# Kernel tuning notes

Measured on AMD Instinct MI355X. Metric: run time of the kernel, lower is better.

## Reference

```python
import jax, jax.numpy as jnp
import numpy as np

B, NE, NN, L = 64, 256, 1024, 512
F_IN, HID = 128, 128
VOCAB = 50000
ALPHA = 0.2
NEG = -9.0e15


def _leaky(z):
    return jnp.where(z >= 0, z, ALPHA * z)


def hga_layer(x, adj, W, W2, W3, a, a2, wc, transfer, concat):
    # x: [B, NN, Fin], adj: [B, NE, NN] (hyperedge incidence)
    O = W2.shape[1]
    x4 = x @ W2                      # [B, NN, O]
    if transfer:
        x = x @ W                    # [B, NN, O]
    # node->edge attention: score depends only on node k (query is shared word_context)
    s0 = wc[0] @ a[:O, 0]            # scalar
    e1 = _leaky(x4 @ a[O:, 0] + s0)  # [B, NN]
    e1 = jnp.broadcast_to(e1[:, None, :], adj.shape)          # [B, NE, NN]
    att_edge = jax.nn.softmax(jnp.where(adj > 0, e1, NEG), axis=2)
    edge = att_edge @ x              # [B, NE, O]
    edge4 = edge @ W3                # [B, NE, O]
    # edge->node attention: query = node feat x4[k], key = edge feat edge4[j]
    e2 = _leaky((x4 @ a2[:O, 0])[:, None, :] + (edge4 @ a2[O:, 0])[:, :, None])  # [B, NE, NN]
    att_node = jax.nn.softmax(jnp.where(adj > 0, e2, NEG).transpose(0, 2, 1), axis=2)  # [B, NN, NE]
    node = att_node @ edge           # [B, NN, O]
    return jax.nn.elu(node) if concat else node


def setup_inputs() -> dict:
    key = jax.random.key(0)
    ks = jax.random.split(key, 16)
    stdv = 1.0 / np.sqrt(HID)
    u = lambda k, shape: jax.random.uniform(k, shape, jnp.float32, -stdv, stdv)
    inp = {
        "items": jax.random.randint(ks[0], (B, NN), 0, VOCAB),
        "alias_inputs": jax.random.randint(ks[1], (B, L), 0, NN),
        "node_masks": jnp.ones((B, L), jnp.float32),
        "adj": jax.random.randint(ks[2], (B, NE, NN), 0, 2).astype(jnp.float32),
        "emb": jax.random.normal(ks[3], (VOCAB, F_IN), jnp.float32),
        # layer 1 (transfer=False, concat=True)
        "w2_1": u(ks[4], (F_IN, HID)),
        "w3_1": u(ks[5], (HID, HID)),
        "a_1": u(ks[6], (2 * HID, 1)),
        "a2_1": u(ks[7], (2 * HID, 1)),
        "wc_1": u(ks[8], (1, HID)),
        # layer 2 (transfer=True, concat=False)
        "w_2": u(ks[9], (HID, HID)),
        "w2_2": u(ks[10], (HID, HID)),
        "w3_2": u(ks[11], (HID, HID)),
        "a_2": u(ks[12], (2 * HID, 1)),
        "a2_2": u(ks[13], (2 * HID, 1)),
        "wc_2": u(ks[14], (1, HID)),
        "ln_g": jnp.ones((HID,), jnp.float32),
        "ln_b": jnp.zeros((HID,), jnp.float32),
    }
    return inp


def reference(items, alias_inputs, node_masks, adj, emb,
              w2_1, w3_1, a_1, a2_1, wc_1,
              w_2, w2_2, w3_2, a_2, a2_2, wc_2,
              ln_g, ln_b):
    hidden = emb[items]                                        # [B, NN, F]
    x = hga_layer(hidden, adj, None, w2_1, w3_1, a_1, a2_1, wc_1,
                  transfer=False, concat=True)
    x = hga_layer(x, adj, w_2, w2_2, w3_2, a_2, a2_2, wc_2,
                  transfer=True, concat=False)                 # [B, NN, HID]
    seq = jnp.take_along_axis(x, alias_inputs[:, :, None], axis=1)  # [B, L, HID]
    m = node_masks[:, :, None]
    h = seq * m
    b = jnp.sum(h * m, axis=-2) / jnp.sum(node_masks, -1, keepdims=True)  # [B, HID]
    mu = jnp.mean(b, -1, keepdims=True)
    var = jnp.mean((b - mu) ** 2, -1, keepdims=True)
    return (b - mu) / jnp.sqrt(var + 1e-6) * ln_g + ln_b
```

## Files before the change

kernel.cpp:

```cpp
#include <hip/hip_runtime.h>
#include <hip/hip_bf16.h>

typedef __hip_bfloat16 bf16;
typedef __attribute__((ext_vector_type(8))) unsigned short u16x8;
typedef __attribute__((ext_vector_type(4))) unsigned short u16x4;
typedef __attribute__((ext_vector_type(4))) float f32x4;
typedef __attribute__((ext_vector_type(8))) short bf16x8;
typedef __attribute__((ext_vector_type(16))) unsigned char u8x16;

#define B_   64
#define NE_  256
#define NN_  1024
#define L_   512
#define HID_ 128
#define ALPHA_ 0.2f

__device__ __forceinline__ float bfu(unsigned short u){
  unsigned int x = ((unsigned int)u) << 16;
  union { unsigned int i; float f; } c; c.i = x; return c.f;
}
__device__ __forceinline__ unsigned short f2b(float f){
  bf16 h = __float2bfloat16(f);
  union { bf16 b; unsigned short u; } c; c.b = h; return c.u;
}
__device__ __forceinline__ int swz(int r, int c){ return (c ^ (r & 3) ^ ((r >> 2) & 3)) & 3; }

__global__ void k_consts(const float* w2_1, const float* w3_1,
                         const float* a_1, const float* a2_1, const float* wc_1,
                         const float* w2_2, const float* w3_2,
                         const float* a_2, const float* a2_2, const float* wc_2,
                         const float* w_2,
                         float* consts, unsigned short* W2T)
{
  int blk = blockIdx.x, t = threadIdx.x;
  __shared__ float red[128];
  if (blk < 6) {
    const float* M; const float* v;
    switch (blk) {
      case 0: M = w2_1; v = a_1  + 128; break;
      case 1: M = w2_1; v = a2_1;       break;
      case 2: M = w3_1; v = a2_1 + 128; break;
      case 3: M = w2_2; v = a_2  + 128; break;
      case 4: M = w2_2; v = a2_2;       break;
      default: M = w3_2; v = a2_2 + 128; break;
    }
    float acc = 0.f;
    for (int o = 0; o < 128; ++o) acc += M[t*128 + o] * v[o];
    consts[blk*128 + t] = acc;
  } else if (blk < 8) {
    const float* wc = (blk == 6) ? wc_1 : wc_2;
    const float* a  = (blk == 6) ? a_1  : a_2;
    red[t] = wc[t] * a[t];
    __syncthreads();
    for (int s = 64; s > 0; s >>= 1) { if (t < s) red[t] += red[t + s]; __syncthreads(); }
    if (t == 0) consts[768 + (blk - 6)] = red[0];
  } else {
    for (int k = 0; k < 128; ++k) W2T[t*128 + k] = f2b(w_2[k*128 + t]);
  }
}

__global__ void k_prep(const float* __restrict__ adj,
                       unsigned char* __restrict__ ADJB, unsigned char* __restrict__ ADJT)
{
  __shared__ unsigned char tile[64][68];
  int b  = blockIdx.z;
  int e0 = blockIdx.y * 64;
  int n0 = blockIdx.x * 64;
  int t  = threadIdx.x;
  int lr = t >> 2, lc0 = (t & 3) * 16;
  const float* src = adj + ((long)b*NE_ + e0 + lr)*NN_ + n0 + lc0;
  u8x16 ov;
  #pragma unroll
  for (int j = 0; j < 16; j += 4) {
    f32x4 v = *(const f32x4*)(src + j);
    #pragma unroll
    for (int k = 0; k < 4; ++k) {
      unsigned char u = (v[k] != 0.f) ? 1 : 0;
      ov[j+k] = u; tile[lr][lc0+j+k] = u;
    }
  }
  *(u8x16*)(ADJB + ((long)b*NE_ + e0 + lr)*NN_ + n0 + lc0) = ov;
  __syncthreads();
  u8x16 o;
  #pragma unroll
  for (int j = 0; j < 16; ++j) o[j] = tile[lc0 + j][lr];
  *(u8x16*)(ADJT + ((long)b*NN_ + n0 + lr)*NE_ + e0 + lc0) = o;
}

template<int SRCBF>
__global__ void k_fproj(const float* __restrict__ srcF, const unsigned short* __restrict__ srcB,
                        const int* __restrict__ gitems,
                        const float* __restrict__ consts, int layer,
                        float* __restrict__ w1, float* __restrict__ f1,
                        unsigned short* __restrict__ YT)
{
  __shared__ float ce1s[128], cf1s[128];
  __shared__ __attribute__((aligned(16))) unsigned short T[64][132];
  int b = blockIdx.y, n0 = blockIdx.x * 64, t = threadIdx.x;
  if (t < 128) { ce1s[t] = consts[layer*384 + t]; cf1s[t] = consts[layer*384 + 128 + t]; }
  __syncthreads();
  int r = t >> 2, h0 = (t & 3) * 32;
  long row = (long)b*NN_ + n0 + r;
  float s0 = consts[768 + layer];
  float xv[32];
  if (SRCBF) {
    const unsigned short* sp = srcB + row*HID_ + h0;
    #pragma unroll
    for (int j = 0; j < 32; j += 8) {
      u16x8 v = *(const u16x8*)(sp + j);
      #pragma unroll
      for (int k = 0; k < 8; ++k) xv[j+k] = bfu(v[k]);
    }
  } else {
    const float* sp = srcF + (long)gitems[row]*HID_ + h0;
    #pragma unroll
    for (int j = 0; j < 32; j += 4) {
      f32x4 v = *(const f32x4*)(sp + j);
      #pragma unroll
      for (int k = 0; k < 4; ++k) xv[j+k] = v[k];
    }
  }
  float p1 = 0.f, p2 = 0.f;
  #pragma unroll
  for (int j = 0; j < 32; ++j) { p1 += xv[j]*ce1s[h0+j]; p2 += xv[j]*cf1s[h0+j]; }
  p1 += __shfl_xor(p1, 1, 4); p1 += __shfl_xor(p1, 2, 4);
  p2 += __shfl_xor(p2, 1, 4); p2 += __shfl_xor(p2, 2, 4);
  float z = p1 + s0; z = (z >= 0.f) ? z : ALPHA_*z;
  float w = __expf(z);
  if ((t & 3) == 0) { w1[row] = w; f1[row] = p2; }
  #pragma unroll
  for (int j = 0; j < 32; j += 4) {
    u16x4 o;
    #pragma unroll
    for (int k = 0; k < 4; ++k) o[k] = f2b(w * xv[j+k]);
    *(u16x4*)&T[r][h0+j] = o;
  }
  __syncthreads();
  int h = t >> 1, nh = (t & 1) * 32;
  unsigned short* dst = YT + ((long)b*HID_ + h)*NN_ + n0 + nh;
  #pragma unroll
  for (int j = 0; j < 32; j += 8) {
    u16x8 o;
    #pragma unroll
    for (int k = 0; k < 8; ++k) o[k] = T[nh+j+k][h];
    *(u16x8*)&dst[j] = o;
  }
}

template<int TRANSFER>
__global__ __launch_bounds__(256) void k_gemm_edge(
    const unsigned char* __restrict__ ADJB,
    const unsigned short* __restrict__ YT,
    const float* __restrict__ w1v,
    const float* __restrict__ consts, int layer,
    const unsigned short* __restrict__ W2T,
    unsigned short* __restrict__ ET,
    float* __restrict__ f2o)
{
  __shared__ __attribute__((aligned(16))) unsigned short SM[12288];
  __shared__ float dsum[64];
  const int id = blockIdx.x;
  const int b = id & 63;
  const long e0 = (long)(id >> 6) * 64;
  const int t = threadIdx.x;
  const int lane = t & 63;
  const int w = t >> 6, wm = w >> 1, wn = w & 1;
  const int r4 = t >> 2, c4 = t & 3;
  const int lr = lane & 15, g = lane >> 4;

  f32x4 acc[2][4];
  #pragma unroll
  for (int i = 0; i < 2; ++i)
    #pragma unroll
    for (int j = 0; j < 4; ++j) acc[i][j] = (f32x4){0.f,0.f,0.f,0.f};

  const unsigned char*  Ab = ADJB + ((long)b*NE_ + e0 + r4)*NN_;
  const unsigned short* Bb = YT + (long)b*HID_*NN_;
  const float*          wb = w1v + (long)b*NN_;

  unsigned long aw; u16x8 bv0, bv1; f32x4 wv0, wv1;
  float dot = 0.f;

  auto stage = [&](int kc) {
    aw  = *(const unsigned long*)(Ab + kc + c4*8);
    wv0 = *(const f32x4*)(wb + kc + c4*8);
    wv1 = *(const f32x4*)(wb + kc + c4*8 + 4);
    bv0 = *(const u16x8*)(Bb + (long)r4*NN_ + kc + c4*8);
    bv1 = *(const u16x8*)(Bb + (long)(64+r4)*NN_ + kc + c4*8);
  };
  auto commit = [&](int buf) {
    u16x8 av;
    #pragma unroll
    for (int j = 0; j < 8; ++j) {
      unsigned int by = (unsigned int)(aw >> (8*j)) & 0xffu;
      av[j] = by ? (unsigned short)0x3F80 : (unsigned short)0;
      float wj = (j < 4) ? wv0[j] : wv1[j-4];
      dot += by ? wj : 0.f;
    }
    *(u16x8*)&SM[buf*2048 + r4*32 + swz(r4,c4)*8] = av;
    *(u16x8*)&SM[4096 + buf*4096 + r4*32 + swz(r4,c4)*8] = bv0;
    *(u16x8*)&SM[4096 + buf*4096 + (64+r4)*32 + swz(64+r4,c4)*8] = bv1;
  };

  stage(0); commit(0);
  int cur = 0;
  const int NIT = NN_/32;
  for (int it = 0; it < NIT; ++it) {
    __syncthreads();
    if (it+1 < NIT) stage((it+1)*32);
    const unsigned short* AsB = &SM[cur*2048];
    const unsigned short* BsB = &SM[4096 + cur*4096];
    bf16x8 af[2], bfr[4];
    #pragma unroll
    for (int mt = 0; mt < 2; ++mt) {
      int r = wm*32 + mt*16 + lr;
      af[mt] = *(const bf16x8*)&AsB[r*32 + swz(r,g)*8];
    }
    #pragma unroll
    for (int nt = 0; nt < 4; ++nt) {
      int n = wn*64 + nt*16 + lr;
      bfr[nt] = *(const bf16x8*)&BsB[n*32 + swz(n,g)*8];
    }
    #pragma unroll
    for (int mt = 0; mt < 2; ++mt)
      #pragma unroll
      for (int nt = 0; nt < 4; ++nt)
        acc[mt][nt] = __builtin_amdgcn_mfma_f32_16x16x32_bf16(af[mt], bfr[nt], acc[mt][nt], 0, 0, 0);
    if (it+1 < NIT) { commit(cur^1); cur ^= 1; }
  }
  dot += __shfl_down(dot, 2, 4); dot += __shfl_down(dot, 1, 4);
  if ((lane & 3) == 0) dsum[r4] = dot;
  __syncthreads();
  #pragma unroll
  for (int mt = 0; mt < 2; ++mt)
    #pragma unroll
    for (int nt = 0; nt < 4; ++nt) {
      int col = wn*64 + nt*16 + lr;
      #pragma unroll
      for (int q = 0; q < 4; ++q) {
        int rl = wm*32 + mt*16 + g*4 + q;
        SM[rl*136 + col] = f2b(acc[mt][nt][q] / dsum[rl]);
      }
    }
  __syncthreads();
  if (TRANSFER) {
    f32x4 acc2[2][4];
    #pragma unroll
    for (int i = 0; i < 2; ++i)
      #pragma unroll
      for (int j = 0; j < 4; ++j) acc2[i][j] = (f32x4){0.f,0.f,0.f,0.f};
    #pragma unroll
    for (int kc2 = 0; kc2 < 4; ++kc2) {
      bf16x8 af[2], bfr[4];
      #pragma unroll
      for (int mt = 0; mt < 2; ++mt) {
        int r = wm*32 + mt*16 + lr;
        af[mt] = *(const bf16x8*)&SM[r*136 + kc2*32 + g*8];
      }
      #pragma unroll
      for (int nt = 0; nt < 4; ++nt) {
        int n = wn*64 + nt*16 + lr;
        bfr[nt] = *(const bf16x8*)(W2T + n*128 + kc2*32 + g*8);
      }
      #pragma unroll
      for (int mt = 0; mt < 2; ++mt)
        #pragma unroll
        for (int nt = 0; nt < 4; ++nt)
          acc2[mt][nt] = __builtin_amdgcn_mfma_f32_16x16x32_bf16(af[mt], bfr[nt], acc2[mt][nt], 0, 0, 0);
    }
    __syncthreads();
    #pragma unroll
    for (int mt = 0; mt < 2; ++mt)
      #pragma unroll
      for (int nt = 0; nt < 4; ++nt) {
        int col = wn*64 + nt*16 + lr;
        #pragma unroll
        for (int q = 0; q < 4; ++q) {
          int rl = wm*32 + mt*16 + g*4 + q;
          SM[rl*136 + col] = f2b(acc2[mt][nt][q]);
        }
      }
    __syncthreads();
  }
  {
    const float* cf2 = consts + layer*384 + 256;
    int r = t >> 2, h0 = (t & 3) * 32;
    float p = 0.f;
    #pragma unroll
    for (int j = 0; j < 32; ++j) p += bfu(SM[r*136 + h0 + j]) * cf2[h0 + j];
    p += __shfl_down(p, 2, 4); p += __shfl_down(p, 1, 4);
    if ((t & 3) == 0) f2o[(long)b*NE_ + e0 + r] = p;
  }
  {
    int h = t >> 1, eh = (t & 1) * 32;
    unsigned short* dst = ET + ((long)b*HID_ + h)*NE_ + e0 + eh;
    #pragma unroll
    for (int j = 0; j < 32; j += 8) {
      u16x8 o;
      #pragma unroll
      for (int k = 0; k < 8; ++k) o[k] = SM[(eh+j+k)*136 + h];
      *(u16x8*)&dst[j] = o;
    }
  }
}

template<int EPI>
__global__ __launch_bounds__(256, 2) void k_gemm_att(
    const unsigned char* __restrict__ ADJT,
    const unsigned short* __restrict__ ET,
    const float* __restrict__ f1v, const float* __restrict__ f2v,
    unsigned short* __restrict__ X2,
    const float* __restrict__ wcount, float* __restrict__ pooled)
{
  __shared__ __attribute__((aligned(16))) unsigned short SM[12288];
  __shared__ float dsum[64];
  __shared__ float colsum[128];
  const int id = blockIdx.x;
  const int b = id & 63;
  const long m0 = (long)(id >> 6) * 64;
  const int t = threadIdx.x;
  const int lane = t & 63;
  const int w = t >> 6, wm = w >> 1, wn = w & 1;
  const int r4 = t >> 2, c4 = t & 3;
  const int lr = lane & 15, g = lane >> 4;

  f32x4 acc[2][4];
  #pragma unroll
  for (int i = 0; i < 2; ++i)
    #pragma unroll
    for (int j = 0; j < 4; ++j) acc[i][j] = (f32x4){0.f,0.f,0.f,0.f};

  const float f1r = f1v[(long)b*NN_ + m0 + r4];
  const unsigned char*  Ab = ADJT + ((long)b*NN_ + m0 + r4)*NE_;
  const unsigned short* Bb = ET + (long)b*HID_*NE_;
  const float* f2p = f2v + (long)b*NE_;

  unsigned long aw; u16x8 bv0, bv1; f32x4 fv0, fv1;
  float dot = 0.f;

  auto stage = [&](int kc) {
    aw  = *(const unsigned long*)(Ab + kc + c4*8);
    fv0 = *(const f32x4*)(f2p + kc + c4*8);
    fv1 = *(const f32x4*)(f2p + kc + c4*8 + 4);
    bv0 = *(const u16x8*)(Bb + (long)r4*NE_ + kc + c4*8);
    bv1 = *(const u16x8*)(Bb + (long)(64+r4)*NE_ + kc + c4*8);
  };
  auto commit = [&](int buf) {
    u16x8 av;
    #pragma unroll
    for (int j = 0; j < 8; ++j) {
      unsigned int by = (unsigned int)(aw >> (8*j)) & 0xffu;
      float z = f1r + ((j < 4) ? fv0[j] : fv1[j-4]);
      z = (z >= 0.f) ? z : ALPHA_ * z;
      float wt = by ? __expf(z) : 0.f;
      unsigned short us = f2b(wt);
      av[j] = us; dot += bfu(us);
    }
    *(u16x8*)&SM[buf*2048 + r4*32 + swz(r4,c4)*8] = av;
    *(u16x8*)&SM[4096 + buf*4096 + r4*32 + swz(r4,c4)*8] = bv0;
    *(u16x8*)&SM[4096 + buf*4096 + (64+r4)*32 + swz(64+r4,c4)*8] = bv1;
  };

  stage(0); commit(0);
  int cur = 0;
  const int NIT = NE_/32;
  for (int it = 0; it < NIT; ++it) {
    __syncthreads();
    if (it+1 < NIT) stage((it+1)*32);
    const unsigned short* AsB = &SM[cur*2048];
    const unsigned short* BsB = &SM[4096 + cur*4096];
    bf16x8 af[2], bfr[4];
    #pragma unroll
    for (int mt = 0; mt < 2; ++mt) {
      int r = wm*32 + mt*16 + lr;
      af[mt] = *(const bf16x8*)&AsB[r*32 + swz(r,g)*8];
    }
    #pragma unroll
    for (int nt = 0; nt < 4; ++nt) {
      int n = wn*64 + nt*16 + lr;
      bfr[nt] = *(const bf16x8*)&BsB[n*32 + swz(n,g)*8];
    }
    #pragma unroll
    for (int mt = 0; mt < 2; ++mt)
      #pragma unroll
      for (int nt = 0; nt < 4; ++nt)
        acc[mt][nt] = __builtin_amdgcn_mfma_f32_16x16x32_bf16(af[mt], bfr[nt], acc[mt][nt], 0, 0, 0);
    if (it+1 < NIT) { commit(cur^1); cur ^= 1; }
  }
  dot += __shfl_down(dot, 2, 4); dot += __shfl_down(dot, 1, 4);
  if ((lane & 3) == 0) dsum[r4] = dot;
  if (EPI == 2 && t < 128) colsum[t] = 0.f;
  __syncthreads();

  if (EPI == 1) {
    #pragma unroll
    for (int mt = 0; mt < 2; ++mt)
      #pragma unroll
      for (int nt = 0; nt < 4; ++nt) {
        int col = wn*64 + nt*16 + lr;
        #pragma unroll
        for (int q = 0; q < 4; ++q) {
          int rl = wm*32 + mt*16 + g*4 + q;
          float v = acc[mt][nt][q] / dsum[rl];
          v = (v > 0.f) ? v : expm1f(v);
          X2[(long)b*NN_*HID_ + (m0 + rl)*HID_ + col] = f2b(v);
        }
      }
  } else {
    float psum[4] = {0.f, 0.f, 0.f, 0.f};
    #pragma unroll
    for (int mt = 0; mt < 2; ++mt)
      #pragma unroll
      for (int q = 0; q < 4; ++q) {
        int rl = wm*32 + mt*16 + g*4 + q;
        float wc = wcount[(long)b*NN_ + m0 + rl];
        float inv = wc / dsum[rl];
        #pragma unroll
        for (int nt = 0; nt < 4; ++nt) psum[nt] += inv * acc[mt][nt][q];
      }
    #pragma unroll
    for (int nt = 0; nt < 4; ++nt) atomicAdd(&colsum[wn*64 + nt*16 + lr], psum[nt]);
    __syncthreads();
    if (t < 128) atomicAdd(&pooled[(long)b*HID_ + t], colsum[t]);
  }
}

__global__ void k_zero(float* __restrict__ p, int n)
{
  int i = blockIdx.x*256 + threadIdx.x;
  if (i < n) p[i] = 0.f;
}

__global__ void k_wcount(const int* __restrict__ alias, const float* __restrict__ masks,
                         float* __restrict__ wcount, float* __restrict__ msum)
{
  int b = blockIdx.x, t = threadIdx.x;
  float m = masks[b*L_ + t];
  int idx = alias[b*L_ + t];
  atomicAdd(&wcount[(long)b*NN_ + idx], m*m);
  float s = m;
  #pragma unroll
  for (int sh = 32; sh > 0; sh >>= 1) s += __shfl_down(s, sh);
  __shared__ float red[8];
  if ((t & 63) == 0) red[t >> 6] = s;
  __syncthreads();
  if (t == 0) { float tot = 0.f; for (int i = 0; i < 8; ++i) tot += red[i]; msum[b] = tot; }
}

__global__ void k_ln(const float* __restrict__ pooled, const float* __restrict__ msum,
                     const float* __restrict__ ln_g, const float* __restrict__ ln_b,
                     float* __restrict__ out)
{
  int b = blockIdx.x, t = threadIdx.x;
  __shared__ float sr[2];
  float bv = pooled[b*HID_ + t] / msum[b];
  int lane = t & 63;
  float p = bv;
  #pragma unroll
  for (int s = 32; s > 0; s >>= 1) p += __shfl_xor(p, s);
  if (lane == 0) sr[t >> 6] = p;
  __syncthreads();
  float mu = (sr[0] + sr[1]) * (1.f / HID_);
  float dv = bv - mu;
  p = dv * dv;
  #pragma unroll
  for (int s = 32; s > 0; s >>= 1) p += __shfl_xor(p, s);
  __syncthreads();
  if (lane == 0) sr[t >> 6] = p;
  __syncthreads();
  float var = (sr[0] + sr[1]) * (1.f / HID_);
  out[b*HID_ + t] = dv / sqrtf(var + 1e-6f) * ln_g[t] + ln_b[t];
}

extern "C" void kernel_launch(void* const* d_in, const int* in_sizes, int n_in,
                              void* d_out, int out_size, void* d_ws, size_t ws_size,
                              hipStream_t stream)
{
  const int*   items = (const int*)d_in[0];
  const int*   alias = (const int*)d_in[1];
  const float* masks = (const float*)d_in[2];
  const float* adj   = (const float*)d_in[3];
  const float* emb   = (const float*)d_in[4];
  const float* w2_1  = (const float*)d_in[5];
  const float* w3_1  = (const float*)d_in[6];
  const float* a_1   = (const float*)d_in[7];
  const float* a2_1  = (const float*)d_in[8];
  const float* wc_1  = (const float*)d_in[9];
  const float* w_2   = (const float*)d_in[10];
  const float* w2_2  = (const float*)d_in[11];
  const float* w3_2  = (const float*)d_in[12];
  const float* a_2   = (const float*)d_in[13];
  const float* a2_2  = (const float*)d_in[14];
  const float* wc_2  = (const float*)d_in[15];
  const float* ln_g  = (const float*)d_in[16];
  const float* ln_b  = (const float*)d_in[17];
  float* out = (float*)d_out;

  char* ws = (char*)d_ws;
  size_t off = 0;
  auto alloc = [&](size_t bytes) -> void* {
    void* p = ws + off; off += (bytes + 255) / 256 * 256; return p;
  };
  unsigned char*  ADJB = (unsigned char*) alloc((size_t)B_*NE_*NN_);
  unsigned char*  ADJT = (unsigned char*) alloc((size_t)B_*NN_*NE_);
  unsigned short* YT   = (unsigned short*)alloc((size_t)B_*HID_*NN_*2);
  unsigned short* ET   = (unsigned short*)alloc((size_t)B_*HID_*NE_*2);
  unsigned short* X2BF = (unsigned short*)alloc((size_t)B_*NN_*HID_*2);
  float* wcount= (float*)alloc((size_t)B_*NN_*4);
  float* pooled= (float*)alloc((size_t)B_*HID_*4);
  float* w1    = (float*)alloc((size_t)B_*NN_*4);
  float* f1    = (float*)alloc((size_t)B_*NN_*4);
  float* f2    = (float*)alloc((size_t)B_*NE_*4);
  float* msum  = (float*)alloc(B_*4);
  float* consts= (float*)alloc(772*4);
  unsigned short* W2T = (unsigned short*)alloc((size_t)HID_*HID_*2);
  if (off > ws_size) return;

  const int kZeroN = B_*NN_ + B_*HID_;

  k_consts<<<9, 128, 0, stream>>>(w2_1, w3_1, a_1, a2_1, wc_1, w2_2, w3_2, a_2, a2_2, wc_2,
                                  w_2, consts, W2T);
  k_zero<<<(kZeroN + 255)/256, 256, 0, stream>>>(wcount, kZeroN);
  k_wcount<<<B_, L_, 0, stream>>>(alias, masks, wcount, msum);
  k_prep<<<dim3(NN_/64, NE_/64, B_), 256, 0, stream>>>(adj, ADJB, ADJT);

  k_fproj<0><<<dim3(NN_/64, B_), 256, 0, stream>>>(emb, nullptr, items, consts, 0, w1, f1, YT);
  k_gemm_edge<0><<<B_*(NE_/64), 256, 0, stream>>>(ADJB, YT, w1, consts, 0, W2T, ET, f2);
  k_gemm_att<1><<<B_*(NN_/64), 256, 0, stream>>>(ADJT, ET, f1, f2, X2BF, nullptr, nullptr);

  k_fproj<1><<<dim3(NN_/64, B_), 256, 0, stream>>>(nullptr, X2BF, nullptr, consts, 1, w1, f1, YT);
  k_gemm_edge<1><<<B_*(NE_/64), 256, 0, stream>>>(ADJB, YT, w1, consts, 1, W2T, ET, f2);
  k_gemm_att<2><<<B_*(NN_/64), 256, 0, stream>>>(ADJT, ET, f1, f2, nullptr, wcount, pooled);

  k_ln<<<B_, HID_, 0, stream>>>(pooled, msum, ln_g, ln_b, out);
}
```

Baseline: 140.3 us.

## Bit-pack adjacency masks and fuse layer-2 projection into attention epilogue

Adjacency incidence is stored as packed bitmasks instead of one byte per entry, shrinking the mask traffic in the prep kernel and both GEMM stages. The layer-2 feature projection (weights, f1 scores, transposed weighted features) is computed directly in the layer-1 node-attention epilogue from shared memory, removing the intermediate bf16 node tensor round trip and one kernel launch. This adds an extra shared-memory pass and syncs to the epilogue, and it uses separate w1/f1 buffers per layer.

```diff
diff --git a/kernel.cpp b/kernel.cpp
--- a/kernel.cpp
+++ b/kernel.cpp
@@ -6,7 +6,6 @@
 typedef __attribute__((ext_vector_type(4))) unsigned short u16x4;
 typedef __attribute__((ext_vector_type(4))) float f32x4;
 typedef __attribute__((ext_vector_type(8))) short bf16x8;
-typedef __attribute__((ext_vector_type(16))) unsigned char u8x16;
 
 #define B_   64
 #define NE_  256
@@ -60,65 +59,70 @@
 }
 
 __global__ void k_prep(const float* __restrict__ adj,
-                       unsigned char* __restrict__ ADJB, unsigned char* __restrict__ ADJT)
+                       unsigned long long* __restrict__ ADJBb,
+                       unsigned long long* __restrict__ ADJTb)
 {
   __shared__ unsigned char tile[64][68];
+  __shared__ unsigned short pa[64][4];
+  __shared__ unsigned short pt[64][4];
   int b  = blockIdx.z;
   int e0 = blockIdx.y * 64;
   int n0 = blockIdx.x * 64;
   int t  = threadIdx.x;
   int lr = t >> 2, lc0 = (t & 3) * 16;
   const float* src = adj + ((long)b*NE_ + e0 + lr)*NN_ + n0 + lc0;
-  u8x16 ov;
+  unsigned int mA = 0;
   #pragma unroll
   for (int j = 0; j < 16; j += 4) {
     f32x4 v = *(const f32x4*)(src + j);
     #pragma unroll
     for (int k = 0; k < 4; ++k) {
       unsigned char u = (v[k] != 0.f) ? 1 : 0;
-      ov[j+k] = u; tile[lr][lc0+j+k] = u;
-    }
-  }
-  *(u8x16*)(ADJB + ((long)b*NE_ + e0 + lr)*NN_ + n0 + lc0) = ov;
-  __syncthreads();
-  u8x16 o;
-  #pragma unroll
-  for (int j = 0; j < 16; ++j) o[j] = tile[lc0 + j][lr];
-  *(u8x16*)(ADJT + ((long)b*NN_ + n0 + lr)*NE_ + e0 + lc0) = o;
-}
-
-template<int SRCBF>
-__global__ void k_fproj(const float* __restrict__ srcF, const unsigned short* __restrict__ srcB,
-                        const int* __restrict__ gitems,
-                        const float* __restrict__ consts, int layer,
+      tile[lr][lc0+j+k] = u;
+      mA |= ((unsigned int)u) << (j+k);
+    }
+  }
+  pa[lr][t & 3] = (unsigned short)mA;
+  __syncthreads();
+  unsigned int mT = 0;
+  #pragma unroll
+  for (int j = 0; j < 16; ++j) mT |= ((unsigned int)tile[lc0 + j][lr]) << j;
+  pt[lr][t & 3] = (unsigned short)mT;
+  __syncthreads();
+  if (t < 64) {
+    unsigned long long wA = (unsigned long long)pa[t][0]
+                          | ((unsigned long long)pa[t][1] << 16)
+                          | ((unsigned long long)pa[t][2] << 32)
+                          | ((unsigned long long)pa[t][3] << 48);
+    ADJBb[((long)b*NE_ + e0 + t)*(NN_/64) + (n0 >> 6)] = wA;
+    unsigned long long wT = (unsigned long long)pt[t][0]
+                          | ((unsigned long long)pt[t][1] << 16)
+                          | ((unsigned long long)pt[t][2] << 32)
+                          | ((unsigned long long)pt[t][3] << 48);
+    ADJTb[((long)b*NN_ + n0 + t)*(NE_/64) + (e0 >> 6)] = wT;
+  }
+}
+
+__global__ void k_fproj(const float* __restrict__ emb, const int* __restrict__ gitems,
+                        const float* __restrict__ consts,
                         float* __restrict__ w1, float* __restrict__ f1,
                         unsigned short* __restrict__ YT)
 {
   __shared__ float ce1s[128], cf1s[128];
   __shared__ __attribute__((aligned(16))) unsigned short T[64][132];
   int b = blockIdx.y, n0 = blockIdx.x * 64, t = threadIdx.x;
-  if (t < 128) { ce1s[t] = consts[layer*384 + t]; cf1s[t] = consts[layer*384 + 128 + t]; }
+  if (t < 128) { ce1s[t] = consts[t]; cf1s[t] = consts[128 + t]; }
   __syncthreads();
   int r = t >> 2, h0 = (t & 3) * 32;
   long row = (long)b*NN_ + n0 + r;
-  float s0 = consts[768 + layer];
+  float s0 = consts[768];
   float xv[32];
-  if (SRCBF) {
-    const unsigned short* sp = srcB + row*HID_ + h0;
-    #pragma unroll
-    for (int j = 0; j < 32; j += 8) {
-      u16x8 v = *(const u16x8*)(sp + j);
-      #pragma unroll
-      for (int k = 0; k < 8; ++k) xv[j+k] = bfu(v[k]);
-    }
-  } else {
-    const float* sp = srcF + (long)gitems[row]*HID_ + h0;
-    #pragma unroll
-    for (int j = 0; j < 32; j += 4) {
-      f32x4 v = *(const f32x4*)(sp + j);
-      #pragma unroll
-      for (int k = 0; k < 4; ++k) xv[j+k] = v[k];
-    }
+  const float* sp = emb + (long)gitems[row]*HID_ + h0;
+  #pragma unroll
+  for (int j = 0; j < 32; j += 4) {
+    f32x4 v = *(const f32x4*)(sp + j);
+    #pragma unroll
+    for (int k = 0; k < 4; ++k) xv[j+k] = v[k];
   }
   float p1 = 0.f, p2 = 0.f;
   #pragma unroll
@@ -149,7 +153,7 @@
 
 template<int TRANSFER>
 __global__ __launch_bounds__(256) void k_gemm_edge(
-    const unsigned char* __restrict__ ADJB,
+    const unsigned char* __restrict__ ADJ8,
     const unsigned short* __restrict__ YT,
     const float* __restrict__ w1v,
     const float* __restrict__ consts, int layer,
@@ -174,15 +178,15 @@
     #pragma unroll
     for (int j = 0; j < 4; ++j) acc[i][j] = (f32x4){0.f,0.f,0.f,0.f};
 
-  const unsigned char*  Ab = ADJB + ((long)b*NE_ + e0 + r4)*NN_;
+  const unsigned char*  Ab = ADJ8 + ((long)b*NE_ + e0 + r4)*(NN_ >> 3);
   const unsigned short* Bb = YT + (long)b*HID_*NN_;
   const float*          wb = w1v + (long)b*NN_;
 
-  unsigned long aw; u16x8 bv0, bv1; f32x4 wv0, wv1;
+  unsigned int ab; u16x8 bv0, bv1; f32x4 wv0, wv1;
   float dot = 0.f;
 
   auto stage = [&](int kc) {
-    aw  = *(const unsigned long*)(Ab + kc + c4*8);
+    ab  = Ab[(kc >> 3) + c4];
     wv0 = *(const f32x4*)(wb + kc + c4*8);
     wv1 = *(const f32x4*)(wb + kc + c4*8 + 4);
     bv0 = *(const u16x8*)(Bb + (long)r4*NN_ + kc + c4*8);
@@ -192,10 +196,10 @@
     u16x8 av;
     #pragma unroll
     for (int j = 0; j < 8; ++j) {
-      unsigned int by = (unsigned int)(aw >> (8*j)) & 0xffu;
-      av[j] = by ? (unsigned short)0x3F80 : (unsigned short)0;
+      unsigned int bit = (ab >> j) & 1u;
+      av[j] = bit ? (unsigned short)0x3F80 : (unsigned short)0;
       float wj = (j < 4) ? wv0[j] : wv1[j-4];
-      dot += by ? wj : 0.f;
+      dot += bit ? wj : 0.f;
     }
     *(u16x8*)&SM[buf*2048 + r4*32 + swz(r4,c4)*8] = av;
     *(u16x8*)&SM[4096 + buf*4096 + r4*32 + swz(r4,c4)*8] = bv0;
@@ -306,15 +310,17 @@
 
 template<int EPI>
 __global__ __launch_bounds__(256, 2) void k_gemm_att(
-    const unsigned char* __restrict__ ADJT,
+    const unsigned char* __restrict__ ADJ8,
     const unsigned short* __restrict__ ET,
     const float* __restrict__ f1v, const float* __restrict__ f2v,
-    unsigned short* __restrict__ X2,
+    const float* __restrict__ consts,
+    unsigned short* __restrict__ YTout, float* __restrict__ w1o, float* __restrict__ f1o,
     const float* __restrict__ wcount, float* __restrict__ pooled)
 {
   __shared__ __attribute__((aligned(16))) unsigned short SM[12288];
   __shared__ float dsum[64];
   __shared__ float colsum[128];
+  __shared__ float wrow[64];
   const int id = blockIdx.x;
   const int b = id & 63;
   const long m0 = (long)(id >> 6) * 64;
@@ -331,15 +337,15 @@
     for (int j = 0; j < 4; ++j) acc[i][j] = (f32x4){0.f,0.f,0.f,0.f};
 
   const float f1r = f1v[(long)b*NN_ + m0 + r4];
-  const unsigned char*  Ab = ADJT + ((long)b*NN_ + m0 + r4)*NE_;
+  const unsigned char*  Ab = ADJ8 + ((long)b*NN_ + m0 + r4)*(NE_ >> 3);
   const unsigned short* Bb = ET + (long)b*HID_*NE_;
   const float* f2p = f2v + (long)b*NE_;
 
-  unsigned long aw; u16x8 bv0, bv1; f32x4 fv0, fv1;
+  unsigned int ab; u16x8 bv0, bv1; f32x4 fv0, fv1;
   float dot = 0.f;
 
   auto stage = [&](int kc) {
-    aw  = *(const unsigned long*)(Ab + kc + c4*8);
+    ab  = Ab[(kc >> 3) + c4];
     fv0 = *(const f32x4*)(f2p + kc + c4*8);
     fv1 = *(const f32x4*)(f2p + kc + c4*8 + 4);
     bv0 = *(const u16x8*)(Bb + (long)r4*NE_ + kc + c4*8);
@@ -349,10 +355,10 @@
     u16x8 av;
     #pragma unroll
     for (int j = 0; j < 8; ++j) {
-      unsigned int by = (unsigned int)(aw >> (8*j)) & 0xffu;
+      unsigned int bit = (ab >> j) & 1u;
       float z = f1r + ((j < 4) ? fv0[j] : fv1[j-4]);
       z = (z >= 0.f) ? z : ALPHA_ * z;
-      float wt = by ? __expf(z) : 0.f;
+      float wt = bit ? __expf(z) : 0.f;
       unsigned short us = f2b(wt);
       av[j] = us; dot += bfu(us);
     }
@@ -403,9 +409,47 @@
           int rl = wm*32 + mt*16 + g*4 + q;
           float v = acc[mt][nt][q] / dsum[rl];
           v = (v > 0.f) ? v : expm1f(v);
-          X2[(long)b*NN_*HID_ + (m0 + rl)*HID_ + col] = f2b(v);
+          SM[rl*136 + col] = f2b(v);
         }
       }
+    __syncthreads();
+    {
+      const float* ce1 = consts + 384;
+      const float* cf1 = consts + 512;
+      int r = t >> 2, h0 = (t & 3) * 32;
+      float p1 = 0.f, p2 = 0.f;
+      #pragma unroll
+      for (int j = 0; j < 32; ++j) {
+        float xv = bfu(SM[r*136 + h0 + j]);
+        p1 += xv * ce1[h0 + j];
+        p2 += xv * cf1[h0 + j];
+      }
+      p1 += __shfl_down(p1, 2, 4); p1 += __shfl_down(p1, 1, 4);
+      p2 += __shfl_down(p2, 2, 4); p2 += __shfl_down(p2, 1, 4);
+      if ((t & 3) == 0) {
+        float z = p1 + consts[769];
+        z = (z >= 0.f) ? z : ALPHA_ * z;
+        float wv = __expf(z);
+        wrow[r] = wv;
+        w1o[(long)b*NN_ + m0 + r] = wv;
+        f1o[(long)b*NN_ + m0 + r] = p2;
+      }
+    }
+    __syncthreads();
+    {
+      int h = t >> 1, nh = (t & 1) * 32;
+      unsigned short* dst = YTout + ((long)b*HID_ + h)*NN_ + m0 + nh;
+      #pragma unroll
+      for (int j = 0; j < 32; j += 8) {
+        u16x8 o;
+        #pragma unroll
+        for (int k = 0; k < 8; ++k) {
+          int rr = nh + j + k;
+          o[k] = f2b(wrow[rr] * bfu(SM[rr*136 + h]));
+        }
+        *(u16x8*)&dst[j] = o;
+      }
+    }
   } else {
     float psum[4] = {0.f, 0.f, 0.f, 0.f};
     #pragma unroll
@@ -501,15 +545,16 @@
   auto alloc = [&](size_t bytes) -> void* {
     void* p = ws + off; off += (bytes + 255) / 256 * 256; return p;
   };
-  unsigned char*  ADJB = (unsigned char*) alloc((size_t)B_*NE_*NN_);
-  unsigned char*  ADJT = (unsigned char*) alloc((size_t)B_*NN_*NE_);
+  unsigned long long* ADJBb = (unsigned long long*)alloc((size_t)B_*NE_*(NN_/8));
+  unsigned long long* ADJTb = (unsigned long long*)alloc((size_t)B_*NN_*(NE_/8));
   unsigned short* YT   = (unsigned short*)alloc((size_t)B_*HID_*NN_*2);
   unsigned short* ET   = (unsigned short*)alloc((size_t)B_*HID_*NE_*2);
-  unsigned short* X2BF = (unsigned short*)alloc((size_t)B_*NN_*HID_*2);
   float* wcount= (float*)alloc((size_t)B_*NN_*4);
   float* pooled= (float*)alloc((size_t)B_*HID_*4);
-  float* w1    = (float*)alloc((size_t)B_*NN_*4);
-  float* f1    = (float*)alloc((size_t)B_*NN_*4);
+  float* w1L1  = (float*)alloc((size_t)B_*NN_*4);
+  float* f1L1  = (float*)alloc((size_t)B_*NN_*4);
+  float* w1L2  = (float*)alloc((size_t)B_*NN_*4);
+  float* f1L2  = (float*)alloc((size_t)B_*NN_*4);
   float* f2    = (float*)alloc((size_t)B_*NE_*4);
   float* msum  = (float*)alloc(B_*4);
   float* consts= (float*)alloc(772*4);
@@ -522,15 +567,18 @@
                                   w_2, consts, W2T);
   k_zero<<<(kZeroN + 255)/256, 256, 0, stream>>>(wcount, kZeroN);
   k_wcount<<<B_, L_, 0, stream>>>(alias, masks, wcount, msum);
-  k_prep<<<dim3(NN_/64, NE_/64, B_), 256, 0, stream>>>(adj, ADJB, ADJT);
-
-  k_fproj<0><<<dim3(NN_/64, B_), 256, 0, stream>>>(emb, nullptr, items, consts, 0, w1, f1, YT);
-  k_gemm_edge<0><<<B_*(NE_/64), 256, 0, stream>>>(ADJB, YT, w1, consts, 0, W2T, ET, f2);
-  k_gemm_att<1><<<B_*(NN_/64), 256, 0, stream>>>(ADJT, ET, f1, f2, X2BF, nullptr, nullptr);
-
-  k_fproj<1><<<dim3(NN_/64, B_), 256, 0, stream>>>(nullptr, X2BF, nullptr, consts, 1, w1, f1, YT);
-  k_gemm_edge<1><<<B_*(NE_/64), 256, 0, stream>>>(ADJB, YT, w1, consts, 1, W2T, ET, f2);
-  k_gemm_att<2><<<B_*(NN_/64), 256, 0, stream>>>(ADJT, ET, f1, f2, nullptr, wcount, pooled);
+  k_prep<<<dim3(NN_/64, NE_/64, B_), 256, 0, stream>>>(adj, ADJBb, ADJTb);
+
+  k_fproj<<<dim3(NN_/64, B_), 256, 0, stream>>>(emb, items, consts, w1L1, f1L1, YT);
+  k_gemm_edge<0><<<B_*(NE_/64), 256, 0, stream>>>((const unsigned char*)ADJBb, YT, w1L1,
+        consts, 0, W2T, ET, f2);
+  k_gemm_att<1><<<B_*(NN_/64), 256, 0, stream>>>((const unsigned char*)ADJTb, ET, f1L1, f2,
+        consts, YT, w1L2, f1L2, nullptr, nullptr);
+
+  k_gemm_edge<1><<<B_*(NE_/64), 256, 0, stream>>>((const unsigned char*)ADJBb, YT, w1L2,
+        consts, 1, W2T, ET, f2);
+  k_gemm_att<2><<<B_*(NN_/64), 256, 0, stream>>>((const unsigned char*)ADJTb, ET, f1L2, f2,
+        consts, nullptr, nullptr, nullptr, wcount, pooled);
 
   k_ln<<<B_, HID_, 0, stream>>>(pooled, msum, ln_g, ln_b, out);
 }
```

Result: faster. 133.6 us (-4.8%).
